# Kernel optimization log

Hardware: AMD Instinct MI355X
Metric: run time of the kernel (lower is better)

The kernel has to match this reference:

```python
import jax, jax.numpy as jnp
import numpy as np

B, S, D, H = 4, 2048, 1024, 16
HD = D // H
SCALE = float(np.sqrt(HD))

def setup_inputs() -> dict:
    key = jax.random.key(0)
    ks = jax.random.split(key, 6)
    std = 1.0 / np.sqrt(D)
    return {
        "x": jax.random.normal(ks[0], (B, S, D), dtype=jnp.float32),
        "Wq": jax.random.normal(ks[1], (D, D), dtype=jnp.float32) * std,
        "Wk": jax.random.normal(ks[2], (D, D), dtype=jnp.float32) * std,
        "Wv": jax.random.normal(ks[3], (D, D), dtype=jnp.float32) * std,
        "Wo": jax.random.normal(ks[4], (D, D), dtype=jnp.float32) * std,
        "bo": jnp.zeros((D,), dtype=jnp.float32),
    }

def reference(x, Wq, Wk, Wv, Wo, bo):
    b, s, _ = x.shape
    # nn.Linear(y) = y @ W.T ; project then split heads -> [B,H,S,HD]
    def proj(W):
        return (x @ W.T).reshape(b, s, H, HD).transpose(0, 2, 1, 3)
    q, k, v = proj(Wq), proj(Wk), proj(Wv)
    scores = jnp.einsum("bhqd,bhkd->bhqk", q, k) / SCALE
    causal = jnp.triu(jnp.ones((s, s), dtype=bool), k=1)
    scores = jnp.where(causal[None, None, :, :], -jnp.inf, scores)
    attn = jax.nn.softmax(scores, axis=-1)  # dropout is identity in eval mode
    out = jnp.einsum("bhqk,bhkd->bhqd", attn, v)
    out = out.transpose(0, 2, 1, 3).reshape(b, s, D)
    return out @ Wo.T + bo
```

## Files before the change

kernel.cpp:

```cpp
#include <hip/hip_runtime.h>
#include <hip/hip_bf16.h>

constexpr int Sc = 2048, Dc = 1024;

typedef __attribute__((ext_vector_type(8))) short bf16x8;
typedef __attribute__((ext_vector_type(4))) short short4v;
typedef __attribute__((ext_vector_type(4))) float f32x4;
typedef __attribute__((ext_vector_type(16))) float f32x16;

static __device__ __forceinline__ short f2bf(float f) {
  __hip_bfloat16 h = __float2bfloat16(f);
  short s; __builtin_memcpy(&s, &h, 2);
  return s;
}

static __device__ __forceinline__ unsigned int cvtpk(float lo, float hi) {
  unsigned int r;
  asm("v_cvt_pk_bf16_f32 %0, %1, %2" : "=v"(r) : "v"(lo), "v"(hi));
  return r;
}

typedef __attribute__((address_space(3))) short lds_short_t;

static __device__ __forceinline__ void gload16(const short* g, lds_short_t* l) {
  __builtin_amdgcn_global_load_lds(
      (const __attribute__((address_space(1))) unsigned int*)g,
      (__attribute__((address_space(3))) unsigned int*)l, 16, 0, 0);
}

__global__ __launch_bounds__(256) void cvt_f32_bf16(const float* __restrict__ src,
                                                    short* __restrict__ dst,
                                                    int n4) {
  int i = blockIdx.x * 256 + threadIdx.x;
  if (i >= n4) return;
  float4 v = ((const float4*)src)[i];
  short4v o;
  o.x = f2bf(v.x); o.y = f2bf(v.y); o.z = f2bf(v.z); o.w = f2bf(v.w);
  ((short4v*)dst)[i] = o;
}

__global__ __launch_bounds__(256) void cvt_w4(const float* __restrict__ w0,
                                              const float* __restrict__ w1,
                                              const float* __restrict__ w2,
                                              const float* __restrict__ w3,
                                              short* __restrict__ dst) {
  const int y = blockIdx.y;
  const float* src = (y == 0) ? w0 : (y == 1) ? w1 : (y == 2) ? w2 : w3;
  int i = blockIdx.x * 256 + threadIdx.x;
  float4 v = ((const float4*)src)[i];
  short4v o;
  o.x = f2bf(v.x); o.y = f2bf(v.y); o.z = f2bf(v.z); o.w = f2bf(v.w);
  ((short4v*)(dst))[(size_t)y * 262144 + i] = o;
}

template <int MODE>
__global__ __launch_bounds__(256) void gemm_bk64(
    const short* __restrict__ A, const short* __restrict__ W,
    const float* __restrict__ bias, short* __restrict__ Qb,
    short* __restrict__ Kb, short* __restrict__ Vt, float* __restrict__ outF) {
  __shared__ short As[128 * 64];
  __shared__ short Bs[128 * 64];
  const int tid = threadIdx.x;
  const int m0 = blockIdx.x * 128, n0 = blockIdx.y * 128;
  const int lane = tid & 63, w = tid >> 6;
  const int wr = w >> 1, wc = w & 1;
  const int ll = lane & 15, lh = lane >> 4;

  lds_short_t* As3 = (lds_short_t*)As;
  lds_short_t* Bs3 = (lds_short_t*)Bs;

  const short* Abase[4];
  const short* Wbase[4];
  int dstOff[4];
#pragma unroll
  for (int i = 0; i < 4; ++i) {
    int slot = i * 256 + tid;
    int row = slot >> 3;
    int gp = (slot & 7) ^ (row & 7);
    Abase[i] = A + (size_t)(m0 + row) * 1024 + gp * 8;
    Wbase[i] = W + (size_t)(n0 + row) * 1024 + gp * 8;
    dstOff[i] = (i * 256 + w * 64) * 8;
  }

  f32x4 acc[4][4] = {};

  for (int k0 = 0; k0 < 1024; k0 += 64) {
    __syncthreads();
#pragma unroll
    for (int i = 0; i < 4; ++i) gload16(Abase[i] + k0, As3 + dstOff[i]);
#pragma unroll
    for (int i = 0; i < 4; ++i) gload16(Wbase[i] + k0, Bs3 + dstOff[i]);
    __syncthreads();

    bf16x8 fa[4][2], fb[4][2];
#pragma unroll
    for (int mi = 0; mi < 4; ++mi) {
      int r = wr * 64 + mi * 16 + ll;
#pragma unroll
      for (int kh = 0; kh < 2; ++kh)
        fa[mi][kh] =
            *(const bf16x8*)&As[r * 64 + (((kh * 4 + lh) ^ (ll & 7)) * 8)];
    }
#pragma unroll
    for (int ni = 0; ni < 4; ++ni) {
      int r = wc * 64 + ni * 16 + ll;
#pragma unroll
      for (int kh = 0; kh < 2; ++kh)
        fb[ni][kh] =
            *(const bf16x8*)&Bs[r * 64 + (((kh * 4 + lh) ^ (ll & 7)) * 8)];
    }
#pragma unroll
    for (int mi = 0; mi < 4; ++mi)
#pragma unroll
      for (int ni = 0; ni < 4; ++ni)
#pragma unroll
        for (int kh = 0; kh < 2; ++kh)
          acc[mi][ni] = __builtin_amdgcn_mfma_f32_16x16x32_bf16(
              fa[mi][kh], fb[ni][kh], acc[mi][ni], 0, 0, 0);
  }

#pragma unroll
  for (int mi = 0; mi < 4; ++mi) {
#pragma unroll
    for (int ni = 0; ni < 4; ++ni) {
#pragma unroll
      for (int r = 0; r < 4; ++r) {
        int row = m0 + wr * 64 + mi * 16 + lh * 4 + r;
        int n = n0 + wc * 64 + ni * 16 + ll;
        float v = acc[mi][ni][r];
        if constexpr (MODE == 1) {
          outF[(size_t)row * 1024 + n] = v + bias[n];
        } else {
          if (n < 1024) {
            Qb[(size_t)row * 1024 + n] = f2bf(v * 0.18033688f);
          } else if (n < 2048) {
            Kb[(size_t)row * 1024 + (n - 1024)] = f2bf(v);
          } else {
            int cc = n - 2048, hh = cc >> 6, dd = cc & 63;
            int bb = row >> 11, ss = row & 2047;
            Vt[(size_t)((bb * 16 + hh) * 64 + dd) * 2048 + ss] = f2bf(v);
          }
        }
      }
    }
  }
}

__global__ __launch_bounds__(256, 3) void attn_v7(const short* __restrict__ Q,
                                                  const short* __restrict__ K,
                                                  const short* __restrict__ Vt,
                                                  short* __restrict__ AO) {
  __shared__ short Ks[2][64 * 64];
  __shared__ short Vs[2][64 * 64];
  const int tid = threadIdx.x, lane = tid & 63, w = tid >> 6;
  const int l31 = lane & 31, lh2 = lane >> 5;
  const int id = blockIdx.x;
  const int bh = id & 63;
  const int qs = id >> 6;
  const int jj = qs >> 2;
  const int qb = (jj == 0) ? qs : (jj == 1) ? 19 - qs : (jj == 2) ? qs - 4 : 23 - qs;
  const int b = bh >> 4, h = bh & 15;
  const int q0 = qb * 128;
  const int R = q0 + w * 32;
  const int kw_last = (R + 31) >> 6;
  const int kb_max = (q0 + 127) >> 6;
  const short* Qp = Q + (size_t)b * Sc * Dc + h * 64;
  const short* Kp = K + (size_t)b * Sc * Dc + h * 64;
  const short* Vp = Vt + (size_t)bh * 64 * Sc;

  lds_short_t* Ks3 = (lds_short_t*)Ks;
  lds_short_t* Vs3 = (lds_short_t*)Vs;

  bf16x8 qf[4];
#pragma unroll
  for (int dk = 0; dk < 4; ++dk)
    qf[dk] = *(const bf16x8*)&Qp[(size_t)(R + l31) * Dc + dk * 16 + lh2 * 8];

  const short* Kst[2];
  const short* Vst[2];
  int ldsOff[2];
#pragma unroll
  for (int i = 0; i < 2; ++i) {
    int slot = i * 256 + w * 64 + lane;
    int row = slot >> 3;
    int col = ((slot & 7) ^ (row & 7)) * 8;
    Kst[i] = Kp + (size_t)row * 1024 + col;
    Vst[i] = Vp + (size_t)row * 2048 + col;
    ldsOff[i] = (i * 256 + w * 64) * 8;
  }

  f32x16 o0 = {}, o1 = {};
  float lrun = 0.f;

#pragma unroll
  for (int i = 0; i < 2; ++i) {
    gload16(Kst[i], Ks3 + ldsOff[i]);
    gload16(Vst[i], Vs3 + ldsOff[i]);
  }
  int cur = 0;

  for (int kb = 0; kb <= kb_max; ++kb) {
    __syncthreads();
    if (kb < kb_max) {
      int nb = cur ^ 1;
#pragma unroll
      for (int i = 0; i < 2; ++i) {
        gload16(Kst[i] + (size_t)(kb + 1) * 65536, Ks3 + nb * 4096 + ldsOff[i]);
        gload16(Vst[i] + (kb + 1) * 64, Vs3 + nb * 4096 + ldsOff[i]);
      }
    }

    if (kb <= kw_last) {
      const bool diag = (kb == kw_last);
      const bool skipHi = diag && ((R & 63) == 0);

      f32x16 sv0 = {}, sv1 = {};
      {
        const int row = l31, rx = row & 7;
#pragma unroll
        for (int dk = 0; dk < 4; ++dk) {
          bf16x8 kf =
              *(const bf16x8*)&Ks[cur][row * 64 + (((dk * 2 + lh2) ^ rx) * 8)];
          sv0 = __builtin_amdgcn_mfma_f32_32x32x16_bf16(kf, qf[dk], sv0, 0, 0, 0);
        }
      }
      if (!skipHi) {
        const int row = 32 + l31, rx = row & 7;
#pragma unroll
        for (int dk = 0; dk < 4; ++dk) {
          bf16x8 kf =
              *(const bf16x8*)&Ks[cur][row * 64 + (((dk * 2 + lh2) ^ rx) * 8)];
          sv1 = __builtin_amdgcn_mfma_f32_32x32x16_bf16(kf, qf[dk], sv1, 0, 0, 0);
        }
      }

      float ts = 0.f;
      if (!diag) {
#pragma unroll
        for (int r = 0; r < 16; ++r) {
          float e0 = exp2f(sv0[r]);
          float e1 = exp2f(sv1[r]);
          sv0[r] = e0; sv1[r] = e1;
          ts += e0 + e1;
        }
      } else if (skipHi) {
#pragma unroll
        for (int r = 0; r < 16; ++r) {
          int kl = (r & 3) + 8 * (r >> 2) + 4 * lh2;
          float e = (kl > l31) ? 0.f : exp2f(sv0[r]);
          sv0[r] = e;
          ts += e;
        }
      } else {
#pragma unroll
        for (int r = 0; r < 16; ++r) {
          float e = exp2f(sv0[r]);
          sv0[r] = e;
          ts += e;
        }
#pragma unroll
        for (int r = 0; r < 16; ++r) {
          int kl = (r & 3) + 8 * (r >> 2) + 4 * lh2;
          float e = (kl > l31) ? 0.f : exp2f(sv1[r]);
          sv1[r] = e;
          ts += e;
        }
      }
      lrun += ts;

      short4v pa[8];
#pragma unroll
      for (int t = 0; t < 4; ++t) {
        union { unsigned int u[2]; short4v s; } pk;
        pk.u[0] = cvtpk(sv0[4 * t + 0], sv0[4 * t + 1]);
        pk.u[1] = cvtpk(sv0[4 * t + 2], sv0[4 * t + 3]);
        pa[t] = pk.s;
      }
      if (skipHi) {
        const int r0 = l31, rx0 = r0 & 7;
        const int r1 = 32 + l31, rx1 = r1 & 7;
#pragma unroll
        for (int t = 0; t < 4; ++t) {
          short4v vb0 =
              *(const short4v*)&Vs[cur][r0 * 64 + ((t ^ rx0) * 8) + lh2 * 4];
          o0 = __builtin_amdgcn_mfma_f32_32x32x8bf16_1k(pa[t], vb0, o0, 0, 0, 0);
          short4v vb1 =
              *(const short4v*)&Vs[cur][r1 * 64 + ((t ^ rx1) * 8) + lh2 * 4];
          o1 = __builtin_amdgcn_mfma_f32_32x32x8bf16_1k(pa[t], vb1, o1, 0, 0, 0);
        }
      } else {
#pragma unroll
        for (int t = 0; t < 4; ++t) {
          union { unsigned int u[2]; short4v s; } pk;
          pk.u[0] = cvtpk(sv1[4 * t + 0], sv1[4 * t + 1]);
          pk.u[1] = cvtpk(sv1[4 * t + 2], sv1[4 * t + 3]);
          pa[4 + t] = pk.s;
        }
        const int r0 = l31, rx0 = r0 & 7;
        const int r1 = 32 + l31, rx1 = r1 & 7;
#pragma unroll
        for (int t = 0; t < 8; ++t) {
          short4v vb0 =
              *(const short4v*)&Vs[cur][r0 * 64 + ((t ^ rx0) * 8) + lh2 * 4];
          o0 = __builtin_amdgcn_mfma_f32_32x32x8bf16_1k(pa[t], vb0, o0, 0, 0, 0);
        }
#pragma unroll
        for (int t = 0; t < 8; ++t) {
          short4v vb1 =
              *(const short4v*)&Vs[cur][r1 * 64 + ((t ^ rx1) * 8) + lh2 * 4];
          o1 = __builtin_amdgcn_mfma_f32_32x32x8bf16_1k(pa[t], vb1, o1, 0, 0, 0);
        }
      }
    }
    cur ^= 1;
  }

  float ltot = lrun + __shfl_xor(lrun, 32);
#pragma unroll
  for (int r = 0; r < 16; ++r) {
    int qr = (r & 3) + 8 * (r >> 2) + 4 * lh2;
    float lq = __shfl(ltot, qr);
    float inv = 1.0f / lq;
    int rowg = R + qr;
    AO[((size_t)(b * Sc + rowg)) * Dc + h * 64 + l31] = f2bf(o0[r] * inv);
    AO[((size_t)(b * Sc + rowg)) * Dc + h * 64 + 32 + l31] = f2bf(o1[r] * inv);
  }
}

extern "C" void kernel_launch(void* const* d_in, const int* in_sizes, int n_in,
                              void* d_out, int out_size, void* d_ws,
                              size_t ws_size, hipStream_t stream) {
  const float* x = (const float*)d_in[0];
  const float* Wq = (const float*)d_in[1];
  const float* Wk = (const float*)d_in[2];
  const float* Wv = (const float*)d_in[3];
  const float* Wo = (const float*)d_in[4];
  const float* bo = (const float*)d_in[5];
  float* out = (float*)d_out;

  short* Qb = (short*)d_out;
  short* Kb = Qb + (size_t)8192 * 1024;
  short* xb = (short*)d_ws;
  short* AOb = xb;
  short* Wc = xb + (size_t)8192 * 1024;
  short* Vt = Wc + (size_t)4096 * 1024;

  dim3 blk(256);
  hipLaunchKernelGGL(cvt_f32_bf16, dim3(8192), blk, 0, stream, x, xb, 2097152);
  hipLaunchKernelGGL(cvt_w4, dim3(1024, 4), blk, 0, stream, Wq, Wk, Wv, Wo, Wc);

  hipLaunchKernelGGL((gemm_bk64<0>), dim3(64, 24), blk, 0, stream, xb, Wc,
                     (const float*)nullptr, Qb, Kb, Vt, (float*)nullptr);

  hipLaunchKernelGGL(attn_v7, dim3(1024), blk, 0, stream, Qb, Kb, Vt, AOb);

  hipLaunchKernelGGL((gemm_bk64<1>), dim3(64, 8), blk, 0, stream, AOb,
                     Wc + (size_t)3072 * 1024, bo, (short*)nullptr,
                     (short*)nullptr, (short*)nullptr, out);
}
```

Baseline: 188.1 us.

## Double-buffer LDS tiles in projection GEMMs to overlap loads with MFMA

```diff
diff --git a/kernel.cpp b/kernel.cpp
--- a/kernel.cpp
+++ b/kernel.cpp
@@ -54,20 +54,20 @@
 }
 
 template <int MODE>
-__global__ __launch_bounds__(256) void gemm_bk64(
+__global__ __launch_bounds__(256) void gemm_db(
     const short* __restrict__ A, const short* __restrict__ W,
     const float* __restrict__ bias, short* __restrict__ Qb,
     short* __restrict__ Kb, short* __restrict__ Vt, float* __restrict__ outF) {
-  __shared__ short As[128 * 64];
-  __shared__ short Bs[128 * 64];
+  __shared__ short As[2][128 * 64];
+  __shared__ short Bs[2][128 * 64];
   const int tid = threadIdx.x;
   const int m0 = blockIdx.x * 128, n0 = blockIdx.y * 128;
   const int lane = tid & 63, w = tid >> 6;
   const int wr = w >> 1, wc = w & 1;
   const int ll = lane & 15, lh = lane >> 4;
 
-  lds_short_t* As3 = (lds_short_t*)As;
-  lds_short_t* Bs3 = (lds_short_t*)Bs;
+  lds_short_t* As3 = (lds_short_t*)&As[0][0];
+  lds_short_t* Bs3 = (lds_short_t*)&Bs[0][0];
 
   const short* Abase[4];
   const short* Wbase[4];
@@ -84,13 +84,21 @@
 
   f32x4 acc[4][4] = {};
 
+#pragma unroll
+  for (int i = 0; i < 4; ++i) gload16(Abase[i], As3 + dstOff[i]);
+#pragma unroll
+  for (int i = 0; i < 4; ++i) gload16(Wbase[i], Bs3 + dstOff[i]);
+  int cur = 0;
+
   for (int k0 = 0; k0 < 1024; k0 += 64) {
     __syncthreads();
-#pragma unroll
-    for (int i = 0; i < 4; ++i) gload16(Abase[i] + k0, As3 + dstOff[i]);
-#pragma unroll
-    for (int i = 0; i < 4; ++i) gload16(Wbase[i] + k0, Bs3 + dstOff[i]);
-    __syncthreads();
+    if (k0 < 960) {
+      int nb = (cur ^ 1) * 8192;
+#pragma unroll
+      for (int i = 0; i < 4; ++i) gload16(Abase[i] + k0 + 64, As3 + nb + dstOff[i]);
+#pragma unroll
+      for (int i = 0; i < 4; ++i) gload16(Wbase[i] + k0 + 64, Bs3 + nb + dstOff[i]);
+    }
 
     bf16x8 fa[4][2], fb[4][2];
 #pragma unroll
@@ -99,7 +107,7 @@
 #pragma unroll
       for (int kh = 0; kh < 2; ++kh)
         fa[mi][kh] =
-            *(const bf16x8*)&As[r * 64 + (((kh * 4 + lh) ^ (ll & 7)) * 8)];
+            *(const bf16x8*)&As[cur][r * 64 + (((kh * 4 + lh) ^ (ll & 7)) * 8)];
     }
 #pragma unroll
     for (int ni = 0; ni < 4; ++ni) {
@@ -107,8 +115,9 @@
 #pragma unroll
       for (int kh = 0; kh < 2; ++kh)
         fb[ni][kh] =
-            *(const bf16x8*)&Bs[r * 64 + (((kh * 4 + lh) ^ (ll & 7)) * 8)];
-    }
+            *(const bf16x8*)&Bs[cur][r * 64 + (((kh * 4 + lh) ^ (ll & 7)) * 8)];
+    }
+    __builtin_amdgcn_s_setprio(1);
 #pragma unroll
     for (int mi = 0; mi < 4; ++mi)
 #pragma unroll
@@ -117,6 +126,8 @@
         for (int kh = 0; kh < 2; ++kh)
           acc[mi][ni] = __builtin_amdgcn_mfma_f32_16x16x32_bf16(
               fa[mi][kh], fb[ni][kh], acc[mi][ni], 0, 0, 0);
+    __builtin_amdgcn_s_setprio(0);
+    cur ^= 1;
   }
 
 #pragma unroll
@@ -349,12 +360,12 @@
   hipLaunchKernelGGL(cvt_f32_bf16, dim3(8192), blk, 0, stream, x, xb, 2097152);
   hipLaunchKernelGGL(cvt_w4, dim3(1024, 4), blk, 0, stream, Wq, Wk, Wv, Wo, Wc);
 
-  hipLaunchKernelGGL((gemm_bk64<0>), dim3(64, 24), blk, 0, stream, xb, Wc,
+  hipLaunchKernelGGL((gemm_db<0>), dim3(64, 24), blk, 0, stream, xb, Wc,
                      (const float*)nullptr, Qb, Kb, Vt, (float*)nullptr);
 
   hipLaunchKernelGGL(attn_v7, dim3(1024), blk, 0, stream, Qb, Kb, Vt, AOb);
 
-  hipLaunchKernelGGL((gemm_bk64<1>), dim3(64, 8), blk, 0, stream, AOb,
+  hipLaunchKernelGGL((gemm_db<1>), dim3(64, 8), blk, 0, stream, AOb,
                      Wc + (size_t)3072 * 1024, bo, (short*)nullptr,
                      (short*)nullptr, (short*)nullptr, out);
 }
```

Measured after the change: 181.1 us. 1.04x faster.
